# Kernel tuning notes

Hardware: AMD Instinct MI355X
Metric: run time of the kernel (lower is better)

## Reference

```python
import jax, jax.numpy as jnp
import numpy as np

E = 16       # num_experts
TOP_K = 2
D = 1024     # emb_dim
H = 1024     # moe_hidden_dim
SH = 2048    # shared_expert_hidden_dim
B, S = 2, 2048
W_SCALE = 0.02  # realistic init scale for weights


def setup_inputs() -> dict:
    key = jax.random.key(0)
    ks = jax.random.split(key, 9)
    return {
        "x": jax.random.normal(ks[0], (B, S, D), jnp.float32),
        "gate_w": jax.random.normal(ks[1], (E, D), jnp.float32) * W_SCALE,
        "w_gate": jax.random.normal(ks[2], (E, H, D), jnp.float32) * W_SCALE,
        "w1": jax.random.normal(ks[3], (E, H, D), jnp.float32) * W_SCALE,
        "w2": jax.random.normal(ks[4], (E, D, H), jnp.float32) * W_SCALE,
        "shared_w_gate": jax.random.normal(ks[5], (SH, D), jnp.float32) * W_SCALE,
        "shared_w1": jax.random.normal(ks[6], (SH, D), jnp.float32) * W_SCALE,
        "shared_w2": jax.random.normal(ks[7], (D, SH), jnp.float32) * W_SCALE,
        "shared_gate_w": jax.random.normal(ks[8], (1, D), jnp.float32) * W_SCALE,
    }


def reference(x, gate_w, w_gate, w1, w2, shared_w_gate, shared_w1, shared_w2, shared_gate_w):
    b, s, d = x.shape
    x2d = x.reshape(-1, d)                       # [N, D]
    n = x2d.shape[0]

    # --- router ---
    logits = x2d @ gate_w.T                      # [N, E]
    probs = jax.nn.softmax(logits, axis=-1)
    topk_p, topk_i = jax.lax.top_k(probs, TOP_K)  # [N, K]
    topk_p = topk_p / jnp.sum(topk_p, axis=-1, keepdims=True)

    # combine weights per (token, expert): zero for non-selected experts
    comb = jnp.zeros((n, E), x2d.dtype).at[jnp.arange(n)[:, None], topk_i].add(topk_p)  # [N, E]

    # --- per-expert gated FFN, accumulated via scan (keeps peak memory at [N,H]) ---
    def step(acc, ws):
        wg, wa, wo, cw = ws                      # [H,D], [H,D], [D,H], [N]
        h = (x2d @ wa.T) * jax.nn.silu(x2d @ wg.T)   # [N, H]
        return acc + cw[:, None] * (h @ wo.T), None

    out, _ = jax.lax.scan(step, jnp.zeros_like(x2d), (w_gate, w1, w2, comb.T))

    # --- shared expert path ---
    sh = (x2d @ shared_w1.T) * jax.nn.silu(x2d @ shared_w_gate.T)  # [N, SH]
    shared_out = sh @ shared_w2.T                                  # [N, D]
    sg = jax.nn.sigmoid(x2d @ shared_gate_w.T)                     # [N, 1]
    out = out + sg * shared_out

    return out.reshape(b, s, d)
```

## Files before the change

kernel.cpp:

```cpp
#include <hip/hip_runtime.h>
#include <stdint.h>

#define E_    16
#define TOPK  2
#define D_    1024
#define H_    1024
#define SH_   2048
#define NTOK  4096
#define BK    32
#define NDESC 80
#define RTOK  16

typedef unsigned short u16;
typedef __attribute__((ext_vector_type(8))) __bf16 bf16x8;
typedef __attribute__((ext_vector_type(4))) float  f32x4;

__device__ __forceinline__ u16 f2bf(float f) {
  union { float f; unsigned int u; } v; v.f = f;
  unsigned int u = v.u;
  return (u16)((u + 0x7fffu + ((u >> 16) & 1u)) >> 16);
}

__device__ __forceinline__ void gload16(const void* g, void* l) {
  __builtin_amdgcn_global_load_lds(
      (const __attribute__((address_space(1))) unsigned int*)g,
      (__attribute__((address_space(3))) unsigned int*)l, 16, 0, 0);
}

__device__ __forceinline__ void xcd_swz(int gx, int gy, int* ox, int* oy) {
  int nb  = gx * gy;
  int bid = blockIdx.x + gx * blockIdx.y;
  int l   = bid;
  if ((nb & 7) == 0) l = (bid & 7) * (nb >> 3) + (bid >> 3);
  int x = l / gy;
  *ox = x; *oy = l - x * gy;
}

__global__ __launch_bounds__(256) void cvt_k(const float* __restrict__ src,
                                             u16* __restrict__ dst) {
  int i = blockIdx.x * 256 + threadIdx.x;
  float4 f = ((const float4*)src)[i];
  ushort4 o; o.x = f2bf(f.x); o.y = f2bf(f.y); o.z = f2bf(f.z); o.w = f2bf(f.w);
  ((ushort4*)dst)[i] = o;
}

__global__ __launch_bounds__(256) void router_k(
    const float* __restrict__ x, const float* __restrict__ gate_w,
    const float* __restrict__ shared_gate_w,
    int* __restrict__ topk_e, float* __restrict__ topk_w,
    float* __restrict__ sg, int* __restrict__ counts) {
  __shared__ float xs[RTOK][132];
  __shared__ float lg[RTOK][16];
  __shared__ float sgp[RTOK][16];

  int tid = threadIdx.x;
  int e   = tid >> 4;
  int tt  = tid & 15;
  int t0  = blockIdx.x * RTOK;

  float acc = 0.f, sga = 0.f;
  for (int c = 0; c < D_; c += 128) {
    __syncthreads();
    #pragma unroll
    for (int i = 0; i < 2; i++) {
      int f = i * 256 + tid;
      int r = f >> 5, c4 = f & 31;
      *(float4*)&xs[r][c4 * 4] =
          *(const float4*)&x[(size_t)(t0 + r) * D_ + c + c4 * 4];
    }
    __syncthreads();
    const float* gw = &gate_w[(size_t)e * D_ + c];
    #pragma unroll
    for (int d4 = 0; d4 < 32; d4++) {
      float4 g  = *(const float4*)&gw[d4 * 4];
      float4 xv = *(const float4*)&xs[tt][d4 * 4];
      acc += xv.x * g.x + xv.y * g.y + xv.z * g.z + xv.w * g.w;
    }
    #pragma unroll
    for (int j = 0; j < 8; j += 4) {
      float4 s  = *(const float4*)&shared_gate_w[c + e * 8 + j];
      float4 xv = *(const float4*)&xs[tt][e * 8 + j];
      sga += xv.x * s.x + xv.y * s.y + xv.z * s.z + xv.w * s.w;
    }
  }
  lg[tt][e]  = acc;
  sgp[tt][e] = sga;
  __syncthreads();

  if (tid < RTOK) {
    int t = t0 + tid;
    float l[16];
    #pragma unroll
    for (int k = 0; k < 16; k++) l[k] = lg[tid][k];
    int i0 = 0; float l0 = l[0];
    for (int k = 1; k < 16; k++) if (l[k] > l0) { l0 = l[k]; i0 = k; }
    int i1 = -1; float l1 = -3.4e38f;
    for (int k = 0; k < 16; k++) if (k != i0 && l[k] > l1) { l1 = l[k]; i1 = k; }
    float w0 = 1.f / (1.f + expf(l1 - l0));
    float s = 0.f;
    #pragma unroll
    for (int k = 0; k < 16; k++) s += sgp[tid][k];
    topk_e[2*t] = i0; topk_e[2*t+1] = i1;
    topk_w[2*t] = w0; topk_w[2*t+1] = 1.f - w0;
    sg[t] = 1.f / (1.f + expf(-s));
    atomicAdd(&counts[i0], 1);
    atomicAdd(&counts[i1], 1);
  }
}

__global__ void scan_k(const int* __restrict__ counts, int* __restrict__ offs,
                       int* __restrict__ desc_e, int* __restrict__ desc_m) {
  if (threadIdx.x == 0) {
    int s = 0, n = 0;
    for (int e = 0; e < E_; e++) {
      offs[e] = s;
      for (int m0 = 0; m0 < counts[e]; m0 += 128) {
        desc_e[n] = e; desc_m[n] = m0; n++;
      }
      s += counts[e];
    }
    offs[E_] = s;
    for (; n < NDESC; n++) { desc_e[n] = -1; desc_m[n] = 0; }
  }
}

__global__ __launch_bounds__(256) void scatter_k(
    const int* __restrict__ topk_e, const float* __restrict__ topk_w,
    const int* __restrict__ offs, int* __restrict__ fill,
    int* __restrict__ tok_of, float* __restrict__ w_of) {
  int t = blockIdx.x * 256 + threadIdx.x;
  if (t >= NTOK) return;
  for (int k = 0; k < TOPK; k++) {
    int e = topk_e[2*t+k];
    int p = atomicAdd(&fill[e], 1);
    int slot = offs[e] + p;
    tok_of[slot] = t;
    w_of[slot]   = topk_w[2*t+k];
  }
}

__global__ __launch_bounds__(256, 2) void up_kernel(
    const u16* __restrict__ Xb,
    const u16* __restrict__ Wg_all, const u16* __restrict__ W1_all,
    u16* __restrict__ Hout, int H,
    const int* __restrict__ tok_of,
    const int* __restrict__ offs, const int* __restrict__ counts,
    const int* __restrict__ desc_e, const int* __restrict__ desc_m) {
  int bx, by;
  xcd_swz(gridDim.x, gridDim.y, &bx, &by);

  int e, m0, cnt, pbase;
  if (desc_e) {
    e = desc_e[bx];
    if (e < 0) return;
    m0 = desc_m[bx];
    cnt = counts[e]; pbase = offs[e];
  } else {
    e = 0; m0 = bx * 128; cnt = NTOK; pbase = 0;
  }
  int n0 = by * 128;
  const u16* Wg = Wg_all + (size_t)e * H * D_;
  const u16* W1 = W1_all + (size_t)e * H * D_;

  __shared__ u16 smem[2 * 3 * 4096];

  int tid  = threadIdx.x;
  int lane = tid & 63, wave = tid >> 6;
  int wm = wave & 1, wn = wave >> 1;
  int l16 = lane & 15, quad = lane >> 4;

  int sr = wave * 16 + (lane >> 2);
  int sc = (lane & 3) * 8;

  int gm0 = m0 + sr;      if (gm0 >= cnt) gm0 = cnt - 1;
  int gm1 = m0 + sr + 64; if (gm1 >= cnt) gm1 = cnt - 1;
  int tok0 = tok_of ? tok_of[pbase + gm0] : gm0;
  int tok1 = tok_of ? tok_of[pbase + gm1] : gm1;
  const u16* pa0 = Xb + (size_t)tok0 * D_ + sc;
  const u16* pa1 = Xb + (size_t)tok1 * D_ + sc;
  const u16* pg0 = Wg + (size_t)(n0 + sr) * D_ + sc;
  const u16* pg1 = pg0 + (size_t)64 * D_;
  const u16* pu0 = W1 + (size_t)(n0 + sr) * D_ + sc;
  const u16* pu1 = pu0 + (size_t)64 * D_;

  int lbase = wave * 512;

  f32x4 accg[4][4], accu[4][4];
  f32x4 zero = {0.f, 0.f, 0.f, 0.f};
  #pragma unroll
  for (int i = 0; i < 4; i++)
    #pragma unroll
    for (int j = 0; j < 4; j++) { accg[i][j] = zero; accu[i][j] = zero; }

#define STAGE_UP(b) do {                                            \
    u16* s_ = smem + (b) * 12288 + lbase;                           \
    gload16(pa0, s_);        gload16(pa1, s_ + 2048);               \
    gload16(pg0, s_ + 4096); gload16(pg1, s_ + 6144);               \
    gload16(pu0, s_ + 8192); gload16(pu1, s_ + 10240);              \
    pa0 += BK; pa1 += BK; pg0 += BK; pg1 += BK; pu0 += BK; pu1 += BK; \
  } while (0)

  STAGE_UP(0);
  STAGE_UP(1);
  int buf = 0;
  const int nt = D_ / BK;

  for (int t = 0; t < nt; ++t) {
    if (t + 1 < nt) asm volatile("s_waitcnt vmcnt(6)" ::: "memory");
    else            asm volatile("s_waitcnt vmcnt(0)" ::: "memory");
    __builtin_amdgcn_s_barrier();
    __builtin_amdgcn_sched_barrier(0);

    const u16* base = smem + buf * 12288;
    bf16x8 af[4], gf[4], uf[4];
    #pragma unroll
    for (int i = 0; i < 4; i++) {
      af[i] = *(const bf16x8*)&base[(wm*64 + i*16 + l16)*BK + quad*8];
      gf[i] = *(const bf16x8*)&base[4096 + (wn*64 + i*16 + l16)*BK + quad*8];
      uf[i] = *(const bf16x8*)&base[8192 + (wn*64 + i*16 + l16)*BK + quad*8];
    }
    #pragma unroll
    for (int i = 0; i < 4; i++)
      #pragma unroll
      for (int j = 0; j < 4; j++) {
        accg[i][j] = __builtin_amdgcn_mfma_f32_16x16x32_bf16(af[i], gf[j], accg[i][j], 0, 0, 0);
        accu[i][j] = __builtin_amdgcn_mfma_f32_16x16x32_bf16(af[i], uf[j], accu[i][j], 0, 0, 0);
      }

    __builtin_amdgcn_sched_barrier(0);
    __builtin_amdgcn_s_barrier();
    if (t + 2 < nt) STAGE_UP(buf);
    buf ^= 1;
  }
#undef STAGE_UP

  #pragma unroll
  for (int i = 0; i < 4; i++) {
    #pragma unroll
    for (int r = 0; r < 4; r++) {
      int m = m0 + wm*64 + i*16 + quad*4 + r;
      if (m < cnt) {
        size_t prow = (size_t)(pbase + m) * H;
        #pragma unroll
        for (int j = 0; j < 4; j++) {
          int n = n0 + wn*64 + j*16 + l16;
          float g = accg[i][j][r];
          float u = accu[i][j][r];
          Hout[prow + n] = f2bf(u * (g / (1.f + expf(-g))));
        }
      }
    }
  }
}

__global__ __launch_bounds__(256, 3) void down_kernel(
    const u16* __restrict__ Hbuf, int K,
    const u16* __restrict__ W2_all,
    float* __restrict__ out,
    const int* __restrict__ tok_of, const float* __restrict__ scale,
    const int* __restrict__ offs, const int* __restrict__ counts,
    const int* __restrict__ desc_e, const int* __restrict__ desc_m,
    int atomic_mode) {
  int bx, by;
  xcd_swz(gridDim.x, gridDim.y, &bx, &by);

  int e, m0, cnt, pbase;
  if (desc_e) {
    e = desc_e[bx];
    if (e < 0) return;
    m0 = desc_m[bx];
    cnt = counts[e]; pbase = offs[e];
  } else {
    e = 0; m0 = bx * 128; cnt = NTOK; pbase = 0;
  }
  int n0 = by * 128;
  const u16* W2 = W2_all + (size_t)e * D_ * K;

  __shared__ u16 smem[2 * 2 * 4096];

  int tid  = threadIdx.x;
  int lane = tid & 63, wave = tid >> 6;
  int wm = wave & 1, wn = wave >> 1;
  int l16 = lane & 15, quad = lane >> 4;

  int sr = wave * 16 + (lane >> 2);
  int sc = (lane & 3) * 8;

  int gm0 = m0 + sr;      if (gm0 >= cnt) gm0 = cnt - 1;
  int gm1 = m0 + sr + 64; if (gm1 >= cnt) gm1 = cnt - 1;
  const u16* pa0 = Hbuf + (size_t)(pbase + gm0) * K + sc;
  const u16* pa1 = Hbuf + (size_t)(pbase + gm1) * K + sc;
  const u16* pb0 = W2 + (size_t)(n0 + sr) * K + sc;
  const u16* pb1 = pb0 + (size_t)64 * K;

  int lbase = wave * 512;

  f32x4 acc[4][4];
  f32x4 zero = {0.f, 0.f, 0.f, 0.f};
  #pragma unroll
  for (int i = 0; i < 4; i++)
    #pragma unroll
    for (int j = 0; j < 4; j++) acc[i][j] = zero;

#define STAGE_DN(b) do {                                \
    u16* s_ = smem + (b) * 8192 + lbase;                \
    gload16(pa0, s_);        gload16(pa1, s_ + 2048);   \
    gload16(pb0, s_ + 4096); gload16(pb1, s_ + 6144);   \
    pa0 += BK; pa1 += BK; pb0 += BK; pb1 += BK;         \
  } while (0)

  STAGE_DN(0);
  STAGE_DN(1);
  int buf = 0;
  const int nt = K / BK;

  for (int t = 0; t < nt; ++t) {
    if (t + 1 < nt) asm volatile("s_waitcnt vmcnt(4)" ::: "memory");
    else            asm volatile("s_waitcnt vmcnt(0)" ::: "memory");
    __builtin_amdgcn_s_barrier();
    __builtin_amdgcn_sched_barrier(0);

    const u16* base = smem + buf * 8192;
    bf16x8 af[4], bfr[4];
    #pragma unroll
    for (int i = 0; i < 4; i++) {
      af[i]  = *(const bf16x8*)&base[(wm*64 + i*16 + l16)*BK + quad*8];
      bfr[i] = *(const bf16x8*)&base[4096 + (wn*64 + i*16 + l16)*BK + quad*8];
    }
    #pragma unroll
    for (int i = 0; i < 4; i++)
      #pragma unroll
      for (int j = 0; j < 4; j++)
        acc[i][j] = __builtin_amdgcn_mfma_f32_16x16x32_bf16(af[i], bfr[j], acc[i][j], 0, 0, 0);

    __builtin_amdgcn_sched_barrier(0);
    __builtin_amdgcn_s_barrier();
    if (t + 2 < nt) STAGE_DN(buf);
    buf ^= 1;
  }
#undef STAGE_DN

  #pragma unroll
  for (int i = 0; i < 4; i++) {
    #pragma unroll
    for (int r = 0; r < 4; r++) {
      int m = m0 + wm*64 + i*16 + quad*4 + r;
      if (m < cnt) {
        int p   = pbase + m;
        int tok = tok_of ? tok_of[p] : p;
        float sc2 = scale[p];
        if (atomic_mode) {
          #pragma unroll
          for (int j = 0; j < 4; j++) {
            int n = n0 + wn*64 + j*16 + l16;
            atomicAdd(&out[(size_t)tok * D_ + n], sc2 * acc[i][j][r]);
          }
        } else {
          #pragma unroll
          for (int j = 0; j < 4; j++) {
            int n = n0 + wn*64 + j*16 + l16;
            out[(size_t)tok * D_ + n] = sc2 * acc[i][j][r];
          }
        }
      }
    }
  }
}

extern "C" void kernel_launch(void* const* d_in, const int* in_sizes, int n_in,
                              void* d_out, int out_size, void* d_ws, size_t ws_size,
                              hipStream_t stream) {
  const float* x      = (const float*)d_in[0];
  const float* gate_w = (const float*)d_in[1];
  const float* w_gate = (const float*)d_in[2];
  const float* w1     = (const float*)d_in[3];
  const float* w2     = (const float*)d_in[4];
  const float* sh_wg  = (const float*)d_in[5];
  const float* sh_w1  = (const float*)d_in[6];
  const float* sh_w2  = (const float*)d_in[7];
  const float* sh_gw  = (const float*)d_in[8];
  float* out = (float*)d_out;

  char* ws = (char*)d_ws;
  size_t off = 0;
  u16* xb    = (u16*)(ws + off); off += (size_t)NTOK * D_ * 2;
  u16* h_exp = (u16*)(ws + off); off += (size_t)NTOK * TOPK * H_ * 2;
  u16* h_sh  = (u16*)(ws + off); off += (size_t)NTOK * SH_ * 2;
  u16* wb_g  = (u16*)(ws + off); off += (size_t)E_ * H_ * D_ * 2;
  u16* wb_1  = (u16*)(ws + off); off += (size_t)E_ * H_ * D_ * 2;
  u16* wb_2  = (u16*)(ws + off); off += (size_t)E_ * D_ * H_ * 2;
  u16* sb_g  = (u16*)(ws + off); off += (size_t)SH_ * D_ * 2;
  u16* sb_1  = (u16*)(ws + off); off += (size_t)SH_ * D_ * 2;
  u16* sb_2  = (u16*)(ws + off); off += (size_t)D_ * SH_ * 2;
  int*   tok_of = (int*)  (ws + off); off += NTOK * TOPK * 4;
  float* w_of   = (float*)(ws + off); off += NTOK * TOPK * 4;
  float* sg     = (float*)(ws + off); off += NTOK * 4;
  int*   topk_e = (int*)  (ws + off); off += NTOK * TOPK * 4;
  float* topk_w = (float*)(ws + off); off += NTOK * TOPK * 4;
  int*   counts = (int*)  (ws + off); off += 64;
  int*   offs   = (int*)  (ws + off); off += 128;
  int*   fill   = (int*)  (ws + off); off += 64;
  int*   desc_e = (int*)  (ws + off); off += NDESC * 4;
  int*   desc_m = (int*)  (ws + off); off += NDESC * 4;

  hipMemsetAsync(counts, 0, 256, stream);

  cvt_k<<<dim3(NTOK * D_ / 1024), 256, 0, stream>>>(x, xb);
  cvt_k<<<dim3(E_ * H_ * D_ / 1024), 256, 0, stream>>>(w_gate, wb_g);
  cvt_k<<<dim3(E_ * H_ * D_ / 1024), 256, 0, stream>>>(w1, wb_1);
  cvt_k<<<dim3(E_ * D_ * H_ / 1024), 256, 0, stream>>>(w2, wb_2);
  cvt_k<<<dim3(SH_ * D_ / 1024), 256, 0, stream>>>(sh_wg, sb_g);
  cvt_k<<<dim3(SH_ * D_ / 1024), 256, 0, stream>>>(sh_w1, sb_1);
  cvt_k<<<dim3(D_ * SH_ / 1024), 256, 0, stream>>>(sh_w2, sb_2);

  router_k<<<dim3(NTOK / RTOK), 256, 0, stream>>>(x, gate_w, sh_gw, topk_e, topk_w, sg, counts);
  scan_k<<<dim3(1), 64, 0, stream>>>(counts, offs, desc_e, desc_m);
  scatter_k<<<dim3((NTOK + 255) / 256), 256, 0, stream>>>(topk_e, topk_w, offs, fill, tok_of, w_of);

  up_kernel<<<dim3(NTOK/128, SH_/128), 256, 0, stream>>>(
      xb, sb_g, sb_1, h_sh, SH_, nullptr, nullptr, nullptr, nullptr, nullptr);
  down_kernel<<<dim3(NTOK/128, D_/128), 256, 0, stream>>>(
      h_sh, SH_, sb_2, out, nullptr, sg, nullptr, nullptr, nullptr, nullptr, 0);

  up_kernel<<<dim3(NDESC, H_/128), 256, 0, stream>>>(
      xb, wb_g, wb_1, h_exp, H_, tok_of, offs, counts, desc_e, desc_m);
  down_kernel<<<dim3(NDESC, D_/128), 256, 0, stream>>>(
      h_exp, H_, wb_2, out, tok_of, w_of, offs, counts, desc_e, desc_m, 1);

  (void)in_sizes; (void)n_in; (void)ws_size;
}
```

Baseline: 523.9 us.

## Merge launches: fuse conversions with router, scan with scatter, shared with routed GEMMs

Collapses the seven conversion kernels and the router into a single grid that picks its job from the block index. It also folds scan and scatter into one single-block kernel, and runs the shared-expert and routed-expert up and down GEMMs as one grid each. The aim is to cut launch count and tail idle time between small dependent kernels, and to let the shared and routed work overlap on the CUs. In exchange, the scatter now runs serially on one block, and the output must be zeroed with a memset. The shared-expert down path also switches from plain stores to atomics.

```diff
diff --git a/kernel.cpp b/kernel.cpp
--- a/kernel.cpp
+++ b/kernel.cpp
@@ -10,10 +10,21 @@
 #define BK    32
 #define NDESC 80
 #define RTOK  16
+#define NRBLK (NTOK / RTOK)
+#define NSHUP (NTOK/128 * SH_/128)
+#define NRTUP (NDESC * H_/128)
+#define NSHDN (NTOK/128 * D_/128)
+#define NRTDN (NDESC * D_/128)
 
 typedef unsigned short u16;
 typedef __attribute__((ext_vector_type(8))) __bf16 bf16x8;
 typedef __attribute__((ext_vector_type(4))) float  f32x4;
+
+struct CvtTable {
+  const float* src[7];
+  u16*         dst[7];
+  int          start[8];
+};
 
 __device__ __forceinline__ u16 f2bf(float f) {
   union { float f; unsigned int u; } v; v.f = f;
@@ -27,24 +38,12 @@
       (__attribute__((address_space(3))) unsigned int*)l, 16, 0, 0);
 }
 
-__device__ __forceinline__ void xcd_swz(int gx, int gy, int* ox, int* oy) {
-  int nb  = gx * gy;
-  int bid = blockIdx.x + gx * blockIdx.y;
-  int l   = bid;
-  if ((nb & 7) == 0) l = (bid & 7) * (nb >> 3) + (bid >> 3);
-  int x = l / gy;
-  *ox = x; *oy = l - x * gy;
-}
-
-__global__ __launch_bounds__(256) void cvt_k(const float* __restrict__ src,
-                                             u16* __restrict__ dst) {
-  int i = blockIdx.x * 256 + threadIdx.x;
-  float4 f = ((const float4*)src)[i];
-  ushort4 o; o.x = f2bf(f.x); o.y = f2bf(f.y); o.z = f2bf(f.z); o.w = f2bf(f.w);
-  ((ushort4*)dst)[i] = o;
-}
-
-__global__ __launch_bounds__(256) void router_k(
+__device__ __forceinline__ int swz8(int b, int nb) {
+  return (b & 7) * (nb >> 3) + (b >> 3);
+}
+
+__global__ __launch_bounds__(256) void cvtrouter_k(
+    CvtTable ct,
     const float* __restrict__ x, const float* __restrict__ gate_w,
     const float* __restrict__ shared_gate_w,
     int* __restrict__ topk_e, float* __restrict__ topk_w,
@@ -53,10 +52,23 @@
   __shared__ float lg[RTOK][16];
   __shared__ float sgp[RTOK][16];
 
+  int b   = blockIdx.x;
   int tid = threadIdx.x;
+
+  if (b >= NRBLK) {
+    int cb = b - NRBLK;
+    int s = 0;
+    while (cb >= ct.start[s + 1]) s++;
+    int i = (cb - ct.start[s]) * 256 + tid;
+    float4 f = ((const float4*)ct.src[s])[i];
+    ushort4 o; o.x = f2bf(f.x); o.y = f2bf(f.y); o.z = f2bf(f.z); o.w = f2bf(f.w);
+    ((ushort4*)ct.dst[s])[i] = o;
+    return;
+  }
+
   int e   = tid >> 4;
   int tt  = tid & 15;
-  int t0  = blockIdx.x * RTOK;
+  int t0  = b * RTOK;
 
   float acc = 0.f, sga = 0.f;
   for (int c = 0; c < D_; c += 128) {
@@ -78,9 +90,9 @@
     }
     #pragma unroll
     for (int j = 0; j < 8; j += 4) {
-      float4 s  = *(const float4*)&shared_gate_w[c + e * 8 + j];
+      float4 s2 = *(const float4*)&shared_gate_w[c + e * 8 + j];
       float4 xv = *(const float4*)&xs[tt][e * 8 + j];
-      sga += xv.x * s.x + xv.y * s.y + xv.z * s.z + xv.w * s.w;
+      sga += xv.x * s2.x + xv.y * s2.y + xv.z * s2.z + xv.w * s2.w;
     }
   }
   lg[tt][e]  = acc;
@@ -108,8 +120,11 @@
   }
 }
 
-__global__ void scan_k(const int* __restrict__ counts, int* __restrict__ offs,
-                       int* __restrict__ desc_e, int* __restrict__ desc_m) {
+__global__ __launch_bounds__(256) void scan_scatter_k(
+    const int* __restrict__ counts, int* __restrict__ offs,
+    int* __restrict__ desc_e, int* __restrict__ desc_m,
+    const int* __restrict__ topk_e, const float* __restrict__ topk_w,
+    int* __restrict__ fill, int* __restrict__ tok_of, float* __restrict__ w_of) {
   if (threadIdx.x == 0) {
     int s = 0, n = 0;
     for (int e = 0; e < E_; e++) {
@@ -122,45 +137,47 @@
     offs[E_] = s;
     for (; n < NDESC; n++) { desc_e[n] = -1; desc_m[n] = 0; }
   }
-}
-
-__global__ __launch_bounds__(256) void scatter_k(
-    const int* __restrict__ topk_e, const float* __restrict__ topk_w,
-    const int* __restrict__ offs, int* __restrict__ fill,
-    int* __restrict__ tok_of, float* __restrict__ w_of) {
-  int t = blockIdx.x * 256 + threadIdx.x;
-  if (t >= NTOK) return;
-  for (int k = 0; k < TOPK; k++) {
-    int e = topk_e[2*t+k];
-    int p = atomicAdd(&fill[e], 1);
-    int slot = offs[e] + p;
-    tok_of[slot] = t;
-    w_of[slot]   = topk_w[2*t+k];
-  }
-}
-
-__global__ __launch_bounds__(256, 2) void up_kernel(
+  __syncthreads();
+  for (int t = threadIdx.x; t < NTOK; t += 256) {
+    for (int k = 0; k < TOPK; k++) {
+      int e = topk_e[2*t+k];
+      int p = atomicAdd(&fill[e], 1);
+      int slot = offs[e] + p;
+      tok_of[slot] = t;
+      w_of[slot]   = topk_w[2*t+k];
+    }
+  }
+}
+
+__global__ __launch_bounds__(256, 2) void up_merged(
     const u16* __restrict__ Xb,
-    const u16* __restrict__ Wg_all, const u16* __restrict__ W1_all,
-    u16* __restrict__ Hout, int H,
+    const u16* __restrict__ sWg, const u16* __restrict__ sW1, u16* __restrict__ sHout,
+    const u16* __restrict__ rWg_all, const u16* __restrict__ rW1_all, u16* __restrict__ rHout,
     const int* __restrict__ tok_of,
     const int* __restrict__ offs, const int* __restrict__ counts,
     const int* __restrict__ desc_e, const int* __restrict__ desc_m) {
-  int bx, by;
-  xcd_swz(gridDim.x, gridDim.y, &bx, &by);
-
-  int e, m0, cnt, pbase;
-  if (desc_e) {
-    e = desc_e[bx];
+  int bid = blockIdx.x;
+  const u16 *Wg, *W1; u16* Hout; int Hdim;
+  int m0, cnt, pbase, n0;
+  const int* tof;
+  if (bid < NSHUP) {
+    int l = swz8(bid, NSHUP);
+    int bx = l >> 4, by = l & 15;
+    m0 = bx * 128; cnt = NTOK; pbase = 0; tof = nullptr;
+    Wg = sWg; W1 = sW1; Hout = sHout; Hdim = SH_;
+    n0 = by * 128;
+  } else {
+    int r = bid - NSHUP;
+    int l = swz8(r, NRTUP);
+    int bx = l >> 3, by = l & 7;
+    int e = desc_e[bx];
     if (e < 0) return;
-    m0 = desc_m[bx];
-    cnt = counts[e]; pbase = offs[e];
-  } else {
-    e = 0; m0 = bx * 128; cnt = NTOK; pbase = 0;
-  }
-  int n0 = by * 128;
-  const u16* Wg = Wg_all + (size_t)e * H * D_;
-  const u16* W1 = W1_all + (size_t)e * H * D_;
+    m0 = desc_m[bx]; cnt = counts[e]; pbase = offs[e]; tof = tok_of;
+    Wg = rWg_all + (size_t)e * H_ * D_;
+    W1 = rW1_all + (size_t)e * H_ * D_;
+    Hout = rHout; Hdim = H_;
+    n0 = by * 128;
+  }
 
   __shared__ u16 smem[2 * 3 * 4096];
 
@@ -174,8 +191,8 @@
 
   int gm0 = m0 + sr;      if (gm0 >= cnt) gm0 = cnt - 1;
   int gm1 = m0 + sr + 64; if (gm1 >= cnt) gm1 = cnt - 1;
-  int tok0 = tok_of ? tok_of[pbase + gm0] : gm0;
-  int tok1 = tok_of ? tok_of[pbase + gm1] : gm1;
+  int tok0 = tof ? tof[pbase + gm0] : gm0;
+  int tok1 = tof ? tof[pbase + gm1] : gm1;
   const u16* pa0 = Xb + (size_t)tok0 * D_ + sc;
   const u16* pa1 = Xb + (size_t)tok1 * D_ + sc;
   const u16* pg0 = Wg + (size_t)(n0 + sr) * D_ + sc;
@@ -240,7 +257,7 @@
     for (int r = 0; r < 4; r++) {
       int m = m0 + wm*64 + i*16 + quad*4 + r;
       if (m < cnt) {
-        size_t prow = (size_t)(pbase + m) * H;
+        size_t prow = (size_t)(pbase + m) * Hdim;
         #pragma unroll
         for (int j = 0; j < 4; j++) {
           int n = n0 + wn*64 + j*16 + l16;
@@ -253,28 +270,33 @@
   }
 }
 
-__global__ __launch_bounds__(256, 3) void down_kernel(
-    const u16* __restrict__ Hbuf, int K,
-    const u16* __restrict__ W2_all,
+__global__ __launch_bounds__(256, 3) void down_merged(
+    const u16* __restrict__ sHbuf, const u16* __restrict__ sW2, const float* __restrict__ sg,
+    const u16* __restrict__ rHbuf, const u16* __restrict__ rW2_all, const float* __restrict__ w_of,
     float* __restrict__ out,
-    const int* __restrict__ tok_of, const float* __restrict__ scale,
+    const int* __restrict__ tok_of,
     const int* __restrict__ offs, const int* __restrict__ counts,
-    const int* __restrict__ desc_e, const int* __restrict__ desc_m,
-    int atomic_mode) {
-  int bx, by;
-  xcd_swz(gridDim.x, gridDim.y, &bx, &by);
-
-  int e, m0, cnt, pbase;
-  if (desc_e) {
-    e = desc_e[bx];
+    const int* __restrict__ desc_e, const int* __restrict__ desc_m) {
+  int bid = blockIdx.x;
+  const u16 *Hbuf, *W2; const float* scale;
+  int m0, cnt, pbase, n0, K;
+  const int* tof;
+  if (bid < NSHDN) {
+    int l = swz8(bid, NSHDN);
+    int bx = l >> 3, by = l & 7;
+    m0 = bx * 128; cnt = NTOK; pbase = 0; tof = nullptr;
+    Hbuf = sHbuf; W2 = sW2; scale = sg; K = SH_;
+    n0 = by * 128;
+  } else {
+    int r = bid - NSHDN;
+    int l = swz8(r, NRTDN);
+    int bx = l >> 3, by = l & 7;
+    int e = desc_e[bx];
     if (e < 0) return;
-    m0 = desc_m[bx];
-    cnt = counts[e]; pbase = offs[e];
-  } else {
-    e = 0; m0 = bx * 128; cnt = NTOK; pbase = 0;
-  }
-  int n0 = by * 128;
-  const u16* W2 = W2_all + (size_t)e * D_ * K;
+    m0 = desc_m[bx]; cnt = counts[e]; pbase = offs[e]; tof = tok_of;
+    Hbuf = rHbuf; W2 = rW2_all + (size_t)e * D_ * H_; scale = w_of; K = H_;
+    n0 = by * 128;
+  }
 
   __shared__ u16 smem[2 * 2 * 4096];
 
@@ -347,20 +369,12 @@
       int m = m0 + wm*64 + i*16 + quad*4 + r;
       if (m < cnt) {
         int p   = pbase + m;
-        int tok = tok_of ? tok_of[p] : p;
+        int tok = tof ? tof[p] : p;
         float sc2 = scale[p];
-        if (atomic_mode) {
-          #pragma unroll
-          for (int j = 0; j < 4; j++) {
-            int n = n0 + wn*64 + j*16 + l16;
-            atomicAdd(&out[(size_t)tok * D_ + n], sc2 * acc[i][j][r]);
-          }
-        } else {
-          #pragma unroll
-          for (int j = 0; j < 4; j++) {
-            int n = n0 + wn*64 + j*16 + l16;
-            out[(size_t)tok * D_ + n] = sc2 * acc[i][j][r];
-          }
+        #pragma unroll
+        for (int j = 0; j < 4; j++) {
+          int n = n0 + wn*64 + j*16 + l16;
+          atomicAdd(&out[(size_t)tok * D_ + n], sc2 * acc[i][j][r]);
         }
       }
     }
@@ -404,28 +418,29 @@
   int*   desc_m = (int*)  (ws + off); off += NDESC * 4;
 
   hipMemsetAsync(counts, 0, 256, stream);
-
-  cvt_k<<<dim3(NTOK * D_ / 1024), 256, 0, stream>>>(x, xb);
-  cvt_k<<<dim3(E_ * H_ * D_ / 1024), 256, 0, stream>>>(w_gate, wb_g);
-  cvt_k<<<dim3(E_ * H_ * D_ / 1024), 256, 0, stream>>>(w1, wb_1);
-  cvt_k<<<dim3(E_ * D_ * H_ / 1024), 256, 0, stream>>>(w2, wb_2);
-  cvt_k<<<dim3(SH_ * D_ / 1024), 256, 0, stream>>>(sh_wg, sb_g);
-  cvt_k<<<dim3(SH_ * D_ / 1024), 256, 0, stream>>>(sh_w1, sb_1);
-  cvt_k<<<dim3(D_ * SH_ / 1024), 256, 0, stream>>>(sh_w2, sb_2);
-
-  router_k<<<dim3(NTOK / RTOK), 256, 0, stream>>>(x, gate_w, sh_gw, topk_e, topk_w, sg, counts);
-  scan_k<<<dim3(1), 64, 0, stream>>>(counts, offs, desc_e, desc_m);
-  scatter_k<<<dim3((NTOK + 255) / 256), 256, 0, stream>>>(topk_e, topk_w, offs, fill, tok_of, w_of);
-
-  up_kernel<<<dim3(NTOK/128, SH_/128), 256, 0, stream>>>(
-      xb, sb_g, sb_1, h_sh, SH_, nullptr, nullptr, nullptr, nullptr, nullptr);
-  down_kernel<<<dim3(NTOK/128, D_/128), 256, 0, stream>>>(
-      h_sh, SH_, sb_2, out, nullptr, sg, nullptr, nullptr, nullptr, nullptr, 0);
-
-  up_kernel<<<dim3(NDESC, H_/128), 256, 0, stream>>>(
-      xb, wb_g, wb_1, h_exp, H_, tok_of, offs, counts, desc_e, desc_m);
-  down_kernel<<<dim3(NDESC, D_/128), 256, 0, stream>>>(
-      h_exp, H_, wb_2, out, tok_of, w_of, offs, counts, desc_e, desc_m, 1);
+  hipMemsetAsync(out, 0, (size_t)NTOK * D_ * 4, stream);
+
+  CvtTable ct;
+  const float* srcs[7] = {x, w_gate, w1, w2, sh_wg, sh_w1, sh_w2};
+  u16*         dsts[7] = {xb, wb_g, wb_1, wb_2, sb_g, sb_1, sb_2};
+  int          nblk[7] = {NTOK*D_/1024, E_*H_*D_/1024, E_*H_*D_/1024,
+                          E_*D_*H_/1024, SH_*D_/1024, SH_*D_/1024, D_*SH_/1024};
+  int s = 0;
+  for (int i = 0; i < 7; i++) { ct.src[i] = srcs[i]; ct.dst[i] = dsts[i];
+                                ct.start[i] = s; s += nblk[i]; }
+  ct.start[7] = s;
+
+  cvtrouter_k<<<dim3(NRBLK + s), 256, 0, stream>>>(
+      ct, x, gate_w, sh_gw, topk_e, topk_w, sg, counts);
+  scan_scatter_k<<<dim3(1), 256, 0, stream>>>(
+      counts, offs, desc_e, desc_m, topk_e, topk_w, fill, tok_of, w_of);
+
+  up_merged<<<dim3(NSHUP + NRTUP), 256, 0, stream>>>(
+      xb, sb_g, sb_1, h_sh, wb_g, wb_1, h_exp,
+      tok_of, offs, counts, desc_e, desc_m);
+  down_merged<<<dim3(NSHDN + NRTDN), 256, 0, stream>>>(
+      h_sh, sb_2, sg, h_exp, wb_2, w_of, out,
+      tok_of, offs, counts, desc_e, desc_m);
 
   (void)in_sizes; (void)n_in; (void)ws_size;
 }
```

Measured after the change: 464.6 us. 11.3% less time.
